# Kernel optimization log

Measured on AMD Instinct MI355X. Metric: run time of the kernel, lower is better.

## Reference

```python
import jax, jax.numpy as jnp
import numpy as np

NQ = 6      # num_qubits
DEPTH = 2
OUT = 8     # out_dim
B = 131072

# --- gate helpers: state has shape [B] + [2]*NQ, wire w lives on axis w+1 (wire 0 = MSB, PennyLane order) ---

def _apply_shared(state, U, w):
    # U: [2,2] shared across batch
    s = jnp.moveaxis(state, w + 1, -1)
    s = jnp.einsum('...j,ij->...i', s, U)
    return jnp.moveaxis(s, -1, w + 1)

def _apply_batched(state, U, w):
    # U: [B,2,2] per-sample gate (angle encoding)
    s = jnp.moveaxis(state, w + 1, -1)
    s = jnp.einsum('b...j,bij->b...i', s, U)
    return jnp.moveaxis(s, -1, w + 1)

def _cnot(state, c, t):
    s = jnp.moveaxis(state, (c + 1, t + 1), (-2, -1))
    s = jnp.concatenate([s[..., 0:1, :], s[..., 1:2, ::-1]], axis=-2)
    return jnp.moveaxis(s, (-2, -1), (c + 1, t + 1))

def _ry(a):
    c, s = jnp.cos(a / 2), jnp.sin(a / 2)
    return jnp.stack([jnp.stack([c, -s], -1), jnp.stack([s, c], -1)], -2).astype(jnp.complex64)

def _rz(a):
    e = jnp.exp(-0.5j * a.astype(jnp.complex64))
    z = jnp.zeros_like(e)
    return jnp.stack([jnp.stack([e, z], -1), jnp.stack([z, jnp.conj(e)], -1)], -2)

def _rx(a):
    c = jnp.cos(a / 2).astype(jnp.complex64)
    s = (-1j) * jnp.sin(a / 2).astype(jnp.complex64)
    return jnp.stack([jnp.stack([c, s], -1), jnp.stack([s, c], -1)], -2)


def setup_inputs() -> dict:
    key = jax.random.key(0)
    kx, kt, kp, ko = jax.random.split(key, 4)
    return {
        'x': jax.random.normal(kx, (B, NQ), dtype=jnp.float32),
        'theta': jax.random.normal(kt, (DEPTH, NQ), dtype=jnp.float32) * 0.01,
        'phi': jax.random.normal(kp, (DEPTH, NQ), dtype=jnp.float32) * 0.01,
        'omega': jax.random.normal(ko, (DEPTH, NQ), dtype=jnp.float32) * 0.01,
    }


def reference(x, theta, phi, omega):
    b = x.shape[0]
    feats = jnp.tanh(x) * jnp.float32(np.pi)  # [B, NQ]
    # |0...0> initial state, batched
    state = jnp.zeros((b,) + (2,) * NQ, jnp.complex64).at[(slice(None),) + (0,) * NQ].set(1.0)
    # angle encoding: RY(f_w) on wire w
    for w in range(NQ):
        state = _apply_batched(state, _ry(feats[:, w]), w)
    # entangling layers
    for l in range(DEPTH):
        for w in range(NQ):
            state = _apply_shared(state, _rz(theta[l, w]), w)
            state = _apply_shared(state, _ry(phi[l, w]), w)
            state = _apply_shared(state, _rx(omega[l, w]), w)
        for w in range(NQ):
            state = _cnot(state, w, (w + 1) % NQ)
    # <Z_w> expectation values
    p = state.real ** 2 + state.imag ** 2  # [B] + [2]*NQ
    zs = []
    for w in range(NQ):
        axes = tuple(a for a in range(1, NQ + 1) if a != w + 1)
        pw = p.sum(axes)  # [B, 2]
        zs.append(pw[:, 0] - pw[:, 1])
    z = jnp.stack(zs, -1)  # [B, NQ]
    idx = np.array([k % NQ for k in range(OUT)])  # circuit measures Z(k % num_qubits)
    return z[:, idx]
```

## Files before the change

kernel.cpp:

```cpp
#include <hip/hip_runtime.h>
#include <math.h>

#define NQ 6

typedef _Float16 h8 __attribute__((ext_vector_type(8)));
typedef float f4   __attribute__((ext_vector_type(4)));
typedef float f8v  __attribute__((ext_vector_type(8)));
typedef float f64v __attribute__((ext_vector_type(64)));
typedef unsigned int uint;

__device__ __forceinline__ uint pk2(float a, float b) {
    return __builtin_bit_cast(uint, __builtin_amdgcn_cvt_pkrtz(a, b));
}

__device__ __forceinline__ void build_gates(const float* theta, const float* phi,
                                            const float* omega, int tid,
                                            float (*g)[NQ][8]) {
    if (tid < 2 * NQ) {
        int l = tid / NQ, w = tid % NQ;
        float th = theta[l*NQ+w]*0.5f, ph = phi[l*NQ+w]*0.5f, om = omega[l*NQ+w]*0.5f;
        float st_, ct, sp, cp, so, co;
        sincosf(th, &st_, &ct); sincosf(ph, &sp, &cp); sincosf(om, &so, &co);
        float A00r = cp*ct,  A00i = -cp*st_;
        float A01r = -sp*ct, A01i = -sp*st_;
        float A10r = sp*ct,  A10i = -sp*st_;
        float A11r = cp*ct,  A11i = cp*st_;
        float* G = g[l][w];
        G[0] = co*A00r + so*A10i;  G[1] = co*A00i - so*A10r;
        G[2] = co*A01r + so*A11i;  G[3] = co*A01i - so*A11r;
        G[4] = so*A00i + co*A10r;  G[5] = -so*A00r + co*A10i;
        G[6] = so*A01i + co*A11r;  G[7] = -so*A01r + co*A11i;
    }
}

__global__ __launch_bounds__(64) void qent_prep(
    const float* __restrict__ theta, const float* __restrict__ phi,
    const float* __restrict__ omega, _Float16* __restrict__ W)
{
    __shared__ float g[2][NQ][8];
    const int i = threadIdx.x;
    build_gates(theta, phi, omega, i, g);
    __syncthreads();
    const int j = blockIdx.x;
    float ar = (i == j) ? 1.f : 0.f, ai = 0.f;
    #pragma unroll
    for (int l = 0; l < 2; ++l) {
        #pragma unroll
        for (int w = 0; w < NQ; ++w) {
            const int tb = 1 << (5 - w);
            float pr = __shfl_xor(ar, tb);
            float pi = __shfl_xor(ai, tb);
            const float* G = g[l][w];
            const bool hi = (i & tb) != 0;
            float car = hi ? G[6] : G[0], cai = hi ? G[7] : G[1];
            float cpr = hi ? G[4] : G[2], cpi = hi ? G[5] : G[3];
            float nar = car*ar - cai*ai + cpr*pr - cpi*pi;
            float nai = car*ai + cai*ar + cpr*pi + cpi*pr;
            ar = nar; ai = nai;
        }
        #pragma unroll
        for (int w = 0; w < NQ; ++w) {
            const int cb = 1 << (5 - w), tb = 1 << (5 - ((w + 1) % NQ));
            float pr = __shfl_xor(ar, tb);
            float pi = __shfl_xor(ai, tb);
            if (i & cb) { ar = pr; ai = pi; }
        }
    }
    const int kt = j >> 5, e = j & 7;
    const int nt = i >> 4;
    const int slot = ((j >> 3) & 3) * 16 + (i & 15);
    W[(kt*4 + nt)*512 + slot*8 + e]     = (_Float16)ar;
    W[(8 + kt*4 + nt)*512 + slot*8 + e] = (_Float16)ai;
}

#define MFMA(d, a, b) d = __builtin_amdgcn_mfma_f32_16x16x32_f16((a), (b), (d), 0, 0, 0)
#define LDA(mt, kt) (*(const h8*)(wbase + ((mt)*16 + (lane & 15))*128 + (((((kt)*4) + (lane >> 4)) ^ (lane & 7)) << 4)))

__global__ __launch_bounds__(256, 2) void qent_main(
    const float* __restrict__ x, const _Float16* __restrict__ Wp,
    float* __restrict__ out, int n)
{
    __shared__ f4 ldsbuf[4096];
    char* lds = (char*)ldsbuf;
    const int tid = threadIdx.x;
    const int lane = tid & 63;
    char* wbase = lds + ((tid >> 6) << 14);
    const int gid = blockIdx.x * 256 + tid;

    const h8* Wv = (const h8*)Wp;
    h8 WR00 = Wv[ 0*64+lane], WR01 = Wv[ 1*64+lane], WR02 = Wv[ 2*64+lane], WR03 = Wv[ 3*64+lane];
    h8 WR10 = Wv[ 4*64+lane], WR11 = Wv[ 5*64+lane], WR12 = Wv[ 6*64+lane], WR13 = Wv[ 7*64+lane];
    h8 WI00 = Wv[ 8*64+lane], WI01 = Wv[ 9*64+lane], WI02 = Wv[10*64+lane], WI03 = Wv[11*64+lane];
    h8 WI10 = Wv[12*64+lane], WI11 = Wv[13*64+lane], WI12 = Wv[14*64+lane], WI13 = Wv[15*64+lane];

    const int sidx = (gid < n) ? gid : (n - 1);
    const float2* xr = (const float2*)(x + (size_t)sidx * 6);
    float2 x01 = xr[0], x23 = xr[1], x45 = xr[2];
    f8v CW, SW;
    #pragma unroll
    for (int w = 0; w < 6; ++w) {
        float xv = (w == 0) ? x01.x : (w == 1) ? x01.y : (w == 2) ? x23.x
                 : (w == 3) ? x23.y : (w == 4) ? x45.x : x45.y;
        xv = fminf(fmaxf(xv, -15.f), 15.f);
        float e2 = __expf(2.f * xv);
        float t = (e2 - 1.f) / (e2 + 1.f);
        float a = t * 1.57079632679489662f;
        float sv, cv;
        __sincosf(a, &sv, &cv);
        CW[w] = cv; SW[w] = sv;
    }

    f64v E;
    E[0] = CW[0]; E[1] = SW[0];
    #pragma unroll
    for (int w = 1; w < 6; ++w) {
        #pragma unroll
        for (int k = (1 << w) - 1; k >= 0; --k) {
            float a = E[k];
            E[2*k]   = a * CW[w];
            E[2*k+1] = a * SW[w];
        }
    }

    #pragma unroll
    for (int k = 0; k < 8; ++k) {
        uint4 q;
        q.x = pk2(E[8*k+0], E[8*k+1]);
        q.y = pk2(E[8*k+2], E[8*k+3]);
        q.z = pk2(E[8*k+4], E[8*k+5]);
        q.w = pk2(E[8*k+6], E[8*k+7]);
        *(uint4*)(wbase + lane*128 + ((k ^ (lane & 7)) << 4)) = q;
    }
    __syncthreads();

    h8 A00 = LDA(0,0), A10 = LDA(1,0), A20 = LDA(2,0), A30 = LDA(3,0);
    h8 A01 = LDA(0,1), A11 = LDA(1,1), A21 = LDA(2,1), A31 = LDA(3,1);

    f4 c00={0,0,0,0}, c01={0,0,0,0}, c02={0,0,0,0}, c03={0,0,0,0};
    f4 c10={0,0,0,0}, c11={0,0,0,0}, c12={0,0,0,0}, c13={0,0,0,0};
    f4 c20={0,0,0,0}, c21={0,0,0,0}, c22={0,0,0,0}, c23={0,0,0,0};
    f4 c30={0,0,0,0}, c31={0,0,0,0}, c32={0,0,0,0}, c33={0,0,0,0};
    MFMA(c00,A00,WR00); MFMA(c01,A00,WR01); MFMA(c02,A00,WR02); MFMA(c03,A00,WR03);
    MFMA(c10,A10,WR00); MFMA(c11,A10,WR01); MFMA(c12,A10,WR02); MFMA(c13,A10,WR03);
    MFMA(c20,A20,WR00); MFMA(c21,A20,WR01); MFMA(c22,A20,WR02); MFMA(c23,A20,WR03);
    MFMA(c30,A30,WR00); MFMA(c31,A30,WR01); MFMA(c32,A30,WR02); MFMA(c33,A30,WR03);
    MFMA(c00,A01,WR10); MFMA(c01,A01,WR11); MFMA(c02,A01,WR12); MFMA(c03,A01,WR13);
    MFMA(c10,A11,WR10); MFMA(c11,A11,WR11); MFMA(c12,A11,WR12); MFMA(c13,A11,WR13);
    MFMA(c20,A21,WR10); MFMA(c21,A21,WR11); MFMA(c22,A21,WR12); MFMA(c23,A21,WR13);
    MFMA(c30,A31,WR10); MFMA(c31,A31,WR11); MFMA(c32,A31,WR12); MFMA(c33,A31,WR13);
    f4 p00 = c00*c00, p01 = c01*c01, p02 = c02*c02, p03 = c03*c03;
    f4 p10 = c10*c10, p11 = c11*c11, p12 = c12*c12, p13 = c13*c13;
    f4 p20 = c20*c20, p21 = c21*c21, p22 = c22*c22, p23 = c23*c23;
    f4 p30 = c30*c30, p31 = c31*c31, p32 = c32*c32, p33 = c33*c33;
    c00=(f4){0,0,0,0}; c01=(f4){0,0,0,0}; c02=(f4){0,0,0,0}; c03=(f4){0,0,0,0};
    c10=(f4){0,0,0,0}; c11=(f4){0,0,0,0}; c12=(f4){0,0,0,0}; c13=(f4){0,0,0,0};
    c20=(f4){0,0,0,0}; c21=(f4){0,0,0,0}; c22=(f4){0,0,0,0}; c23=(f4){0,0,0,0};
    c30=(f4){0,0,0,0}; c31=(f4){0,0,0,0}; c32=(f4){0,0,0,0}; c33=(f4){0,0,0,0};
    MFMA(c00,A00,WI00); MFMA(c01,A00,WI01); MFMA(c02,A00,WI02); MFMA(c03,A00,WI03);
    MFMA(c10,A10,WI00); MFMA(c11,A10,WI01); MFMA(c12,A10,WI02); MFMA(c13,A10,WI03);
    MFMA(c20,A20,WI00); MFMA(c21,A20,WI01); MFMA(c22,A20,WI02); MFMA(c23,A20,WI03);
    MFMA(c30,A30,WI00); MFMA(c31,A30,WI01); MFMA(c32,A30,WI02); MFMA(c33,A30,WI03);
    MFMA(c00,A01,WI10); MFMA(c01,A01,WI11); MFMA(c02,A01,WI12); MFMA(c03,A01,WI13);
    MFMA(c10,A11,WI10); MFMA(c11,A11,WI11); MFMA(c12,A11,WI12); MFMA(c13,A11,WI13);
    MFMA(c20,A21,WI10); MFMA(c21,A21,WI11); MFMA(c22,A21,WI12); MFMA(c23,A21,WI13);
    MFMA(c30,A31,WI10); MFMA(c31,A31,WI11); MFMA(c32,A31,WI12); MFMA(c33,A31,WI13);
    p00 += c00*c00; p01 += c01*c01; p02 += c02*c02; p03 += c03*c03;
    p10 += c10*c10; p11 += c11*c11; p12 += c12*c12; p13 += c13*c13;
    p20 += c20*c20; p21 += c21*c21; p22 += c22*c22; p23 += c23*c23;
    p30 += c30*c30; p31 += c31*c31; p32 += c32*c32; p33 += c33*c33;
    __syncthreads();

#define PART(mt, r) { \
        float q0 = p##mt##0[r], q1 = p##mt##1[r], q2 = p##mt##2[r], q3 = p##mt##3[r]; \
        float a_ = q0 + q1, b_ = q2 + q3; \
        int s_ = (mt)*16 + (lane >> 4)*4 + (r); \
        *(f4*)(wbase + s_*256 + ((((lane & 15)) ^ (s_ & 15)) << 4)) = \
            (f4){a_ + b_, a_ - b_, (q0 - q1) + (q2 - q3), 0.f}; \
    }
    PART(0,0) PART(0,1) PART(0,2) PART(0,3)
    PART(1,0) PART(1,1) PART(1,2) PART(1,3)
    PART(2,0) PART(2,1) PART(2,2) PART(2,3)
    PART(3,0) PART(3,1) PART(3,2) PART(3,3)
#undef PART
    __syncthreads();

    float z0=0.f, z1=0.f, z2=0.f, z3=0.f, z4=0.f, z5=0.f;
    #pragma unroll
    for (int c = 0; c < 16; ++c) {
        f4 rec = *(const f4*)(wbase + lane*256 + ((c ^ (lane & 15)) << 4));
        z0 += rec.y; z1 += rec.z;
        float tot = rec.x;
        z2 += (c & 8) ? -tot : tot;
        z3 += (c & 4) ? -tot : tot;
        z4 += (c & 2) ? -tot : tot;
        z5 += (c & 1) ? -tot : tot;
    }
    if (gid < n) {
        float4* o = (float4*)(out + (size_t)gid * 8);
        o[0] = make_float4(z0, z1, z2, z3);
        o[1] = make_float4(z4, z5, z0, z1);
    }
}

extern "C" void kernel_launch(void* const* d_in, const int* in_sizes, int n_in,
                              void* d_out, int out_size, void* d_ws, size_t ws_size,
                              hipStream_t stream) {
    const float* x     = (const float*)d_in[0];
    const float* theta = (const float*)d_in[1];
    const float* phi   = (const float*)d_in[2];
    const float* omega = (const float*)d_in[3];
    float* out = (float*)d_out;
    _Float16* W = (_Float16*)d_ws;
    int n = in_sizes[0] / NQ;
    hipLaunchKernelGGL(qent_prep, dim3(64), dim3(64), 0, stream, theta, phi, omega, W);
    int blocks = (n + 255) / 256;
    hipLaunchKernelGGL(qent_main, dim3(blocks), dim3(256), 0, stream, x, W, out, n);
}
```

Baseline: 15.91 us.

## Fuse unitary-prep and main kernels, folding layer-1 gates into per-sample encoding

Removes the separate prep kernel by having every block build the gate matrices in LDS. The first entangling layer's rotations are folded into the per-sample product state, which becomes complex. Only the second layer is built as a factored MFMA operand, with the CNOT ring applied as a compile-time permutation. The cost is redundant per-block setup work, twice the A-operand data (real and imaginary parts), a complex GEMM with half-sized blocks, and heavy LDS use (~48KB) that limits occupancy.

Result: slower. 20.94 us (+31.6%).

```diff
diff --git a/kernel.cpp b/kernel.cpp
--- a/kernel.cpp
+++ b/kernel.cpp
@@ -2,20 +2,51 @@
 #include <math.h>
 
 #define NQ 6
+#define DIM 64
 
 typedef _Float16 h8 __attribute__((ext_vector_type(8)));
+typedef float f2   __attribute__((ext_vector_type(2)));
 typedef float f4   __attribute__((ext_vector_type(4)));
-typedef float f8v  __attribute__((ext_vector_type(8)));
 typedef float f64v __attribute__((ext_vector_type(64)));
 typedef unsigned int uint;
 
 __device__ __forceinline__ uint pk2(float a, float b) {
     return __builtin_bit_cast(uint, __builtin_amdgcn_cvt_pkrtz(a, b));
 }
-
-__device__ __forceinline__ void build_gates(const float* theta, const float* phi,
-                                            const float* omega, int tid,
-                                            float (*g)[NQ][8]) {
+__device__ __forceinline__ f2 cmul(f2 a, f2 b) {
+    return (f2){a.x * b.x - a.y * b.y, a.x * b.y + a.y * b.x};
+}
+
+struct Perms {
+    int R[DIM];
+    static constexpr int tau(int l, int c) {
+        const int t = (c + 1) % NQ;
+        const int cb = 1 << (5 - c), tb = 1 << (5 - t);
+        return (l & cb) ? (l ^ tb) : l;
+    }
+    static constexpr int ring(int l) {
+        for (int w = NQ - 1; w >= 0; --w) l = tau(l, w);
+        return l;
+    }
+    constexpr Perms() : R() { for (int l = 0; l < DIM; ++l) R[l] = ring(l); }
+};
+constexpr Perms PP;
+
+#define MFMA(d, a, b) d = __builtin_amdgcn_mfma_f32_16x16x32_f16((a), (b), (d), 0, 0, 0)
+
+__global__ __launch_bounds__(128, 2) void qent_fused(
+    const float* __restrict__ x,
+    const float* __restrict__ theta, const float* __restrict__ phi,
+    const float* __restrict__ omega,
+    float* __restrict__ out, int n)
+{
+    __shared__ __align__(16) char lds[49664];
+    const int tid = threadIdx.x;
+    const int lane = tid & 63;
+    char* b1 = lds;
+    char* abase = lds + 16384 + ((tid >> 6) << 14);
+    float* g = (float*)(lds + 49152);
+
     if (tid < 2 * NQ) {
         int l = tid / NQ, w = tid % NQ;
         float th = theta[l*NQ+w]*0.5f, ph = phi[l*NQ+w]*0.5f, om = omega[l*NQ+w]*0.5f;
@@ -25,78 +56,59 @@
         float A01r = -sp*ct, A01i = -sp*st_;
         float A10r = sp*ct,  A10i = -sp*st_;
         float A11r = cp*ct,  A11i = cp*st_;
-        float* G = g[l][w];
+        float* G = g + (l * NQ + w) * 8;
         G[0] = co*A00r + so*A10i;  G[1] = co*A00i - so*A10r;
         G[2] = co*A01r + so*A11i;  G[3] = co*A01i - so*A11r;
         G[4] = so*A00i + co*A10r;  G[5] = -so*A00r + co*A10i;
         G[6] = so*A01i + co*A11r;  G[7] = -so*A01r + co*A11i;
     }
-}
-
-__global__ __launch_bounds__(64) void qent_prep(
-    const float* __restrict__ theta, const float* __restrict__ phi,
-    const float* __restrict__ omega, _Float16* __restrict__ W)
-{
-    __shared__ float g[2][NQ][8];
-    const int i = threadIdx.x;
-    build_gates(theta, phi, omega, i, g);
     __syncthreads();
-    const int j = blockIdx.x;
-    float ar = (i == j) ? 1.f : 0.f, ai = 0.f;
-    #pragma unroll
-    for (int l = 0; l < 2; ++l) {
-        #pragma unroll
-        for (int w = 0; w < NQ; ++w) {
-            const int tb = 1 << (5 - w);
-            float pr = __shfl_xor(ar, tb);
-            float pi = __shfl_xor(ai, tb);
-            const float* G = g[l][w];
-            const bool hi = (i & tb) != 0;
-            float car = hi ? G[6] : G[0], cai = hi ? G[7] : G[1];
-            float cpr = hi ? G[4] : G[2], cpi = hi ? G[5] : G[3];
-            float nar = car*ar - cai*ai + cpr*pr - cpi*pi;
-            float nai = car*ai + cai*ar + cpr*pi + cpi*pr;
-            ar = nar; ai = nai;
-        }
-        #pragma unroll
-        for (int w = 0; w < NQ; ++w) {
-            const int cb = 1 << (5 - w), tb = 1 << (5 - ((w + 1) % NQ));
-            float pr = __shfl_xor(ar, tb);
-            float pi = __shfl_xor(ai, tb);
-            if (i & cb) { ar = pr; ai = pi; }
-        }
-    }
-    const int kt = j >> 5, e = j & 7;
-    const int nt = i >> 4;
-    const int slot = ((j >> 3) & 3) * 16 + (i & 15);
-    W[(kt*4 + nt)*512 + slot*8 + e]     = (_Float16)ar;
-    W[(8 + kt*4 + nt)*512 + slot*8 + e] = (_Float16)ai;
-}
-
-#define MFMA(d, a, b) d = __builtin_amdgcn_mfma_f32_16x16x32_f16((a), (b), (d), 0, 0, 0)
-#define LDA(mt, kt) (*(const h8*)(wbase + ((mt)*16 + (lane & 15))*128 + (((((kt)*4) + (lane >> 4)) ^ (lane & 7)) << 4)))
-
-__global__ __launch_bounds__(256, 2) void qent_main(
-    const float* __restrict__ x, const _Float16* __restrict__ Wp,
-    float* __restrict__ out, int n)
-{
-    __shared__ f4 ldsbuf[4096];
-    char* lds = (char*)ldsbuf;
-    const int tid = threadIdx.x;
-    const int lane = tid & 63;
-    char* wbase = lds + ((tid >> 6) << 14);
-    const int gid = blockIdx.x * 256 + tid;
-
-    const h8* Wv = (const h8*)Wp;
-    h8 WR00 = Wv[ 0*64+lane], WR01 = Wv[ 1*64+lane], WR02 = Wv[ 2*64+lane], WR03 = Wv[ 3*64+lane];
-    h8 WR10 = Wv[ 4*64+lane], WR11 = Wv[ 5*64+lane], WR12 = Wv[ 6*64+lane], WR13 = Wv[ 7*64+lane];
-    h8 WI00 = Wv[ 8*64+lane], WI01 = Wv[ 9*64+lane], WI02 = Wv[10*64+lane], WI03 = Wv[11*64+lane];
-    h8 WI10 = Wv[12*64+lane], WI11 = Wv[13*64+lane], WI12 = Wv[14*64+lane], WI13 = Wv[15*64+lane];
-
+
+    {
+        const int col = tid & 63, h = tid >> 6;
+        const int J = PP.R[col];
+        const float* g2 = g + NQ * 8;
+        f2 T[32];
+        {
+            const float* G = g2 + ((((J >> 5) & 1) * 2 + h) << 1);
+            T[0] = (f2){G[0], G[1]};
+        }
+        #pragma unroll
+        for (int w = 1; w < 6; ++w) {
+            const int bj = (J >> (5 - w)) & 1;
+            const float* Gr = g2 + w * 8 + ((bj * 2) << 1);
+            f2 v0 = (f2){Gr[0], Gr[1]};
+            f2 v1 = (f2){Gr[2], Gr[3]};
+            #pragma unroll
+            for (int k = (1 << (w - 1)) - 1; k >= 0; --k) {
+                f2 a = T[k];
+                T[2*k]   = cmul(a, v0);
+                T[2*k+1] = cmul(a, v1);
+            }
+        }
+        const int nt = col >> 4;
+        #pragma unroll
+        for (int gg = 0; gg < 4; ++gg) {
+            uint4 qr, qi;
+            qr.x = pk2( T[gg*8+0].x,  T[gg*8+1].x);
+            qr.y = pk2( T[gg*8+2].x,  T[gg*8+3].x);
+            qr.z = pk2( T[gg*8+4].x,  T[gg*8+5].x);
+            qr.w = pk2( T[gg*8+6].x,  T[gg*8+7].x);
+            qi.x = pk2(-T[gg*8+0].y, -T[gg*8+1].y);
+            qi.y = pk2(-T[gg*8+2].y, -T[gg*8+3].y);
+            qi.z = pk2(-T[gg*8+4].y, -T[gg*8+5].y);
+            qi.w = pk2(-T[gg*8+6].y, -T[gg*8+7].y);
+            char* pw = b1 + (h * 4 + nt) * 1024 + ((gg * 16 + (col & 15)) << 4);
+            *(uint4*)pw          = qr;
+            *(uint4*)(pw + 8192) = qi;
+        }
+    }
+
+    const int gid = blockIdx.x * 128 + tid;
     const int sidx = (gid < n) ? gid : (n - 1);
     const float2* xr = (const float2*)(x + (size_t)sidx * 6);
     float2 x01 = xr[0], x23 = xr[1], x45 = xr[2];
-    f8v CW, SW;
+    f2 u0[NQ], u1[NQ];
     #pragma unroll
     for (int w = 0; w < 6; ++w) {
         float xv = (w == 0) ? x01.x : (w == 1) ? x01.y : (w == 2) ? x23.x
@@ -107,87 +119,92 @@
         float a = t * 1.57079632679489662f;
         float sv, cv;
         __sincosf(a, &sv, &cv);
-        CW[w] = cv; SW[w] = sv;
-    }
-
-    f64v E;
-    E[0] = CW[0]; E[1] = SW[0];
+        const f2* G2 = (const f2*)(g + w * 8);
+        f2 cc = {cv, cv}, ss = {sv, sv};
+        u0[w] = cc * G2[0] + ss * G2[1];
+        u1[w] = cc * G2[2] + ss * G2[3];
+    }
+    f64v ER, EI;
+    ER[0] = u0[0].x; EI[0] = u0[0].y;
+    ER[1] = u1[0].x; EI[1] = u1[0].y;
     #pragma unroll
     for (int w = 1; w < 6; ++w) {
         #pragma unroll
         for (int k = (1 << w) - 1; k >= 0; --k) {
-            float a = E[k];
-            E[2*k]   = a * CW[w];
-            E[2*k+1] = a * SW[w];
-        }
-    }
-
-    #pragma unroll
-    for (int k = 0; k < 8; ++k) {
-        uint4 q;
-        q.x = pk2(E[8*k+0], E[8*k+1]);
-        q.y = pk2(E[8*k+2], E[8*k+3]);
-        q.z = pk2(E[8*k+4], E[8*k+5]);
-        q.w = pk2(E[8*k+6], E[8*k+7]);
-        *(uint4*)(wbase + lane*128 + ((k ^ (lane & 7)) << 4)) = q;
+            float ar = ER[k], ai = EI[k];
+            ER[2*k]   = ar * u0[w].x - ai * u0[w].y;
+            EI[2*k]   = ar * u0[w].y + ai * u0[w].x;
+            ER[2*k+1] = ar * u1[w].x - ai * u1[w].y;
+            EI[2*k+1] = ar * u1[w].y + ai * u1[w].x;
+        }
+    }
+
+    #pragma unroll
+    for (int c = 0; c < 8; ++c) {
+        uint4 q, q2;
+        q.x  = pk2(ER[PP.R[8*c+0]], ER[PP.R[8*c+1]]);
+        q.y  = pk2(ER[PP.R[8*c+2]], ER[PP.R[8*c+3]]);
+        q.z  = pk2(ER[PP.R[8*c+4]], ER[PP.R[8*c+5]]);
+        q.w  = pk2(ER[PP.R[8*c+6]], ER[PP.R[8*c+7]]);
+        q2.x = pk2(EI[PP.R[8*c+0]], EI[PP.R[8*c+1]]);
+        q2.y = pk2(EI[PP.R[8*c+2]], EI[PP.R[8*c+3]]);
+        q2.z = pk2(EI[PP.R[8*c+4]], EI[PP.R[8*c+5]]);
+        q2.w = pk2(EI[PP.R[8*c+6]], EI[PP.R[8*c+7]]);
+        *(uint4*)(abase + lane*256 + (( c      ^ (lane & 7)) << 4)) = q;
+        *(uint4*)(abase + lane*256 + (((c + 8) ^ (lane & 7)) << 4)) = q2;
     }
     __syncthreads();
 
-    h8 A00 = LDA(0,0), A10 = LDA(1,0), A20 = LDA(2,0), A30 = LDA(3,0);
-    h8 A01 = LDA(0,1), A11 = LDA(1,1), A21 = LDA(2,1), A31 = LDA(3,1);
-
-    f4 c00={0,0,0,0}, c01={0,0,0,0}, c02={0,0,0,0}, c03={0,0,0,0};
-    f4 c10={0,0,0,0}, c11={0,0,0,0}, c12={0,0,0,0}, c13={0,0,0,0};
-    f4 c20={0,0,0,0}, c21={0,0,0,0}, c22={0,0,0,0}, c23={0,0,0,0};
-    f4 c30={0,0,0,0}, c31={0,0,0,0}, c32={0,0,0,0}, c33={0,0,0,0};
-    MFMA(c00,A00,WR00); MFMA(c01,A00,WR01); MFMA(c02,A00,WR02); MFMA(c03,A00,WR03);
-    MFMA(c10,A10,WR00); MFMA(c11,A10,WR01); MFMA(c12,A10,WR02); MFMA(c13,A10,WR03);
-    MFMA(c20,A20,WR00); MFMA(c21,A20,WR01); MFMA(c22,A20,WR02); MFMA(c23,A20,WR03);
-    MFMA(c30,A30,WR00); MFMA(c31,A30,WR01); MFMA(c32,A30,WR02); MFMA(c33,A30,WR03);
-    MFMA(c00,A01,WR10); MFMA(c01,A01,WR11); MFMA(c02,A01,WR12); MFMA(c03,A01,WR13);
-    MFMA(c10,A11,WR10); MFMA(c11,A11,WR11); MFMA(c12,A11,WR12); MFMA(c13,A11,WR13);
-    MFMA(c20,A21,WR10); MFMA(c21,A21,WR11); MFMA(c22,A21,WR12); MFMA(c23,A21,WR13);
-    MFMA(c30,A31,WR10); MFMA(c31,A31,WR11); MFMA(c32,A31,WR12); MFMA(c33,A31,WR13);
-    f4 p00 = c00*c00, p01 = c01*c01, p02 = c02*c02, p03 = c03*c03;
-    f4 p10 = c10*c10, p11 = c11*c11, p12 = c12*c12, p13 = c13*c13;
-    f4 p20 = c20*c20, p21 = c21*c21, p22 = c22*c22, p23 = c23*c23;
-    f4 p30 = c30*c30, p31 = c31*c31, p32 = c32*c32, p33 = c33*c33;
-    c00=(f4){0,0,0,0}; c01=(f4){0,0,0,0}; c02=(f4){0,0,0,0}; c03=(f4){0,0,0,0};
-    c10=(f4){0,0,0,0}; c11=(f4){0,0,0,0}; c12=(f4){0,0,0,0}; c13=(f4){0,0,0,0};
-    c20=(f4){0,0,0,0}; c21=(f4){0,0,0,0}; c22=(f4){0,0,0,0}; c23=(f4){0,0,0,0};
-    c30=(f4){0,0,0,0}; c31=(f4){0,0,0,0}; c32=(f4){0,0,0,0}; c33=(f4){0,0,0,0};
-    MFMA(c00,A00,WI00); MFMA(c01,A00,WI01); MFMA(c02,A00,WI02); MFMA(c03,A00,WI03);
-    MFMA(c10,A10,WI00); MFMA(c11,A10,WI01); MFMA(c12,A10,WI02); MFMA(c13,A10,WI03);
-    MFMA(c20,A20,WI00); MFMA(c21,A20,WI01); MFMA(c22,A20,WI02); MFMA(c23,A20,WI03);
-    MFMA(c30,A30,WI00); MFMA(c31,A30,WI01); MFMA(c32,A30,WI02); MFMA(c33,A30,WI03);
-    MFMA(c00,A01,WI10); MFMA(c01,A01,WI11); MFMA(c02,A01,WI12); MFMA(c03,A01,WI13);
-    MFMA(c10,A11,WI10); MFMA(c11,A11,WI11); MFMA(c12,A11,WI12); MFMA(c13,A11,WI13);
-    MFMA(c20,A21,WI10); MFMA(c21,A21,WI11); MFMA(c22,A21,WI12); MFMA(c23,A21,WI13);
-    MFMA(c30,A31,WI10); MFMA(c31,A31,WI11); MFMA(c32,A31,WI12); MFMA(c33,A31,WI13);
-    p00 += c00*c00; p01 += c01*c01; p02 += c02*c02; p03 += c03*c03;
-    p10 += c10*c10; p11 += c11*c11; p12 += c12*c12; p13 += c13*c13;
-    p20 += c20*c20; p21 += c21*c21; p22 += c22*c22; p23 += c23*c23;
-    p30 += c30*c30; p31 += c31*c31; p32 += c32*c32; p33 += c33*c33;
-    __syncthreads();
-
-#define PART(mt, r) { \
-        float q0 = p##mt##0[r], q1 = p##mt##1[r], q2 = p##mt##2[r], q3 = p##mt##3[r]; \
-        float a_ = q0 + q1, b_ = q2 + q3; \
-        int s_ = (mt)*16 + (lane >> 4)*4 + (r); \
-        *(f4*)(wbase + s_*256 + ((((lane & 15)) ^ (s_ & 15)) << 4)) = \
-            (f4){a_ + b_, a_ - b_, (q0 - q1) + (q2 - q3), 0.f}; \
-    }
-    PART(0,0) PART(0,1) PART(0,2) PART(0,3)
-    PART(1,0) PART(1,1) PART(1,2) PART(1,3)
-    PART(2,0) PART(2,1) PART(2,2) PART(2,3)
-    PART(3,0) PART(3,1) PART(3,2) PART(3,3)
-#undef PART
-    __syncthreads();
+    h8 A[4][4];
+    #pragma unroll
+    for (int mt = 0; mt < 4; ++mt)
+        #pragma unroll
+        for (int kt = 0; kt < 4; ++kt)
+            A[mt][kt] = *(const h8*)(abase + (mt*16 + (lane & 15))*256 +
+                                     (((kt*4 + (lane >> 4)) ^ (lane & 7)) << 4));
+    f4 fr[4][4], fi[4][4];
+    #pragma unroll
+    for (int mt = 0; mt < 4; ++mt)
+        #pragma unroll
+        for (int nt = 0; nt < 4; ++nt) { fr[mt][nt] = (f4){0,0,0,0}; fi[mt][nt] = (f4){0,0,0,0}; }
+    #pragma unroll
+    for (int kt = 0; kt < 4; ++kt) {
+        h8 B0 = *(const h8*)(b1 + (kt*4 + 0)*1024 + lane*16);
+        h8 B1f = *(const h8*)(b1 + (kt*4 + 1)*1024 + lane*16);
+        h8 B2 = *(const h8*)(b1 + (kt*4 + 2)*1024 + lane*16);
+        h8 B3 = *(const h8*)(b1 + (kt*4 + 3)*1024 + lane*16);
+        #pragma unroll
+        for (int mt = 0; mt < 4; ++mt) {
+            MFMA(fr[mt][0], A[mt][kt], B0);
+            MFMA(fr[mt][1], A[mt][kt], B1f);
+            MFMA(fr[mt][2], A[mt][kt], B2);
+            MFMA(fr[mt][3], A[mt][kt], B3);
+            MFMA(fi[mt][0], A[mt][kt^2], B0);
+            MFMA(fi[mt][1], A[mt][kt^2], B1f);
+            MFMA(fi[mt][2], A[mt][kt^2], B2);
+            MFMA(fi[mt][3], A[mt][kt^2], B3);
+        }
+    }
+
+    #pragma unroll
+    for (int mt = 0; mt < 4; ++mt) {
+        #pragma unroll
+        for (int r = 0; r < 4; ++r) {
+            float q0 = fr[mt][0][r]*fr[mt][0][r] + fi[mt][0][r]*fi[mt][0][r];
+            float q1 = fr[mt][1][r]*fr[mt][1][r] + fi[mt][1][r]*fi[mt][1][r];
+            float q2 = fr[mt][2][r]*fr[mt][2][r] + fi[mt][2][r]*fi[mt][2][r];
+            float q3 = fr[mt][3][r]*fr[mt][3][r] + fi[mt][3][r]*fi[mt][3][r];
+            float a_ = q0 + q1, b_ = q2 + q3;
+            int s_ = mt*16 + (lane >> 4)*4 + r;
+            *(f4*)(abase + s_*256 + (((lane & 15) ^ (s_ & 15)) << 4)) =
+                (f4){a_ + b_, a_ - b_, (q0 - q1) + (q2 - q3), 0.f};
+        }
+    }
 
     float z0=0.f, z1=0.f, z2=0.f, z3=0.f, z4=0.f, z5=0.f;
     #pragma unroll
     for (int c = 0; c < 16; ++c) {
-        f4 rec = *(const f4*)(wbase + lane*256 + ((c ^ (lane & 15)) << 4));
+        f4 rec = *(const f4*)(abase + lane*256 + ((c ^ (lane & 15)) << 4));
         z0 += rec.y; z1 += rec.z;
         float tot = rec.x;
         z2 += (c & 8) ? -tot : tot;
@@ -210,9 +227,8 @@
     const float* phi   = (const float*)d_in[2];
     const float* omega = (const float*)d_in[3];
     float* out = (float*)d_out;
-    _Float16* W = (_Float16*)d_ws;
     int n = in_sizes[0] / NQ;
-    hipLaunchKernelGGL(qent_prep, dim3(64), dim3(64), 0, stream, theta, phi, omega, W);
-    int blocks = (n + 255) / 256;
-    hipLaunchKernelGGL(qent_main, dim3(blocks), dim3(256), 0, stream, x, W, out, n);
-}
+    int blocks = (n + 127) / 128;
+    hipLaunchKernelGGL(qent_fused, dim3(blocks), dim3(128), 0, stream,
+                       x, theta, phi, omega, out, n);
+}
```
